# Optimization experiments

Hardware: AMD Instinct MI355X
Metric: run time of the kernel (lower is better)

The kernel has to match this reference:

```python
import jax, jax.numpy as jnp
import numpy as np

B, S, H = 1024, 128, 1024   # batch, seq_len, bert hidden size
E, HID, K, C = 16, 1024, 4, 3  # experts, expert hidden, top_k, num_classes
EPS = 1e-5


def _ln(x, g, b):
    mu = x.mean(-1, keepdims=True)
    var = ((x - mu) ** 2).mean(-1, keepdims=True)
    return (x - mu) / jnp.sqrt(var + EPS) * g + b


def setup_inputs() -> dict:
    key = jax.random.key(0)
    ks = jax.random.split(key, 24)
    n = lambda k, shape, s=0.02: jax.random.normal(k, shape, jnp.float32) * s
    return {
        "hidden_states": jax.random.normal(ks[0], (B, S, H), jnp.float32),
        # original BertClassificationHead
        "Wd": n(ks[1], (H, H)), "bd": jnp.zeros((H,), jnp.float32),
        "Wo": n(ks[2], (H, C)), "bo": jnp.zeros((C,), jnp.float32),
        # router
        "Wr": n(ks[3], (H, E)), "br": jnp.zeros((E,), jnp.float32),
        # stacked experts: Linear(H,HID) -> LN -> GELU -> Linear(HID,HID)
        "We1": n(ks[4], (E, H, HID)), "be1": jnp.zeros((E, HID), jnp.float32),
        "g1": jnp.ones((E, HID), jnp.float32), "beta1": jnp.zeros((E, HID), jnp.float32),
        "We2": n(ks[5], (E, HID, HID)), "be2": jnp.zeros((E, HID), jnp.float32),
        # expert_output_proj
        "Wp": n(ks[6], (HID, C)), "bp": jnp.zeros((C,), jnp.float32),
        # final_classifier: Linear(2C, C) -> LN -> ReLU -> Linear(C, C)
        "Wf1": n(ks[7], (2 * C, C)), "bf1": jnp.zeros((C,), jnp.float32),
        "gf": jnp.ones((C,), jnp.float32), "betaf": jnp.zeros((C,), jnp.float32),
        "Wf2": n(ks[8], (C, C)), "bf2": jnp.zeros((C,), jnp.float32),
    }


def reference(hidden_states, Wd, bd, Wo, bo, Wr, br, We1, be1, g1, beta1,
              We2, be2, Wp, bp, Wf1, bf1, gf, betaf, Wf2, bf2):
    cls = hidden_states[:, 0]                                   # [B,H]
    # original classifier head (dropout = identity in eval)
    original_logits = jnp.tanh(cls @ Wd + bd) @ Wo + bo         # [B,C]
    # router: top-k softmax scattered into dense [B,E] weights
    router_logits = cls @ Wr + br                               # [B,E]
    topk_vals, topk_idx = jax.lax.top_k(router_logits, K)
    topk_probs = jax.nn.softmax(topk_vals, axis=-1)
    routing_weights = jnp.zeros_like(router_logits).at[
        jnp.arange(cls.shape[0])[:, None], topk_idx].set(topk_probs)
    # experts consume mean-pooled sequence (MLPExpert mean over dim=1)
    m = hidden_states.mean(axis=1)                              # [B,H]
    h = jnp.einsum('bh,ehd->bed', m, We1) + be1                 # [B,E,HID]
    h = jax.nn.gelu(_ln(h, g1, beta1), approximate=False)
    h = jnp.einsum('bed,edf->bef', h, We2) + be2                # [B,E,HID]
    expert_logits = h @ Wp + bp                                 # [B,E,C]
    # weighted combine; routing_weights is zero for non-selected experts,
    # so this equals the sparse top-k dispatch of the original loop
    moe_output = jnp.einsum('be,bec->bc', routing_weights, expert_logits)
    combined = jnp.concatenate([original_logits, moe_output], axis=1)  # [B,2C]
    z = _ln(combined @ Wf1 + bf1, gf, betaf)
    return jax.nn.relu(z) @ Wf2 + bf2                           # [B,C]
```

## Files before the change

### kernel.cpp

```cpp
#include <hip/hip_runtime.h>
#include <math.h>

#define B_ 1024
#define S_ 128
#define H_ 1024
#define E_ 16
#define HID_ 1024
#define K_ 4
#define C_ 3
#define EPS_ 1e-5f

#define NB_MEAN 1024
#define NB_WC 4096
#define NB_RT 256
#define NB_BC 4
#define OFF_WC (NB_MEAN)
#define OFF_RT (OFF_WC + NB_WC)
#define OFF_BC (OFF_RT + NB_RT)
#define NB_PREP (OFF_BC + NB_BC)

typedef __attribute__((ext_vector_type(8))) __bf16 bf16x8;
typedef __attribute__((ext_vector_type(4))) float f32x4;
typedef __attribute__((ext_vector_type(4))) float fvec4;
typedef __attribute__((ext_vector_type(4))) unsigned short usvec4;
typedef __attribute__((ext_vector_type(8))) unsigned short usvec8;

__device__ __forceinline__ ushort bf16_rn(float f) {
  unsigned u = __float_as_uint(f);
  u += 0x7FFF + ((u >> 16) & 1);
  return (ushort)(u >> 16);
}
__device__ __forceinline__ float bf16_to_f(ushort h) {
  return __uint_as_float(((unsigned)h) << 16);
}
__device__ __forceinline__ void split2(float f, ushort& h, ushort& l) {
  h = bf16_rn(f);
  l = bf16_rn(f - bf16_to_f(h));
}
__device__ __forceinline__ void gload_lds16(const void* g, void* l) {
  __builtin_amdgcn_global_load_lds((const __attribute__((address_space(1))) void*)g,
                                   (__attribute__((address_space(3))) void*)l, 16, 0, 0);
}
#define DMA_DRAIN() do {                                  \
    asm volatile("s_waitcnt vmcnt(0)" ::: "memory");      \
    __builtin_amdgcn_sched_barrier(0);                    \
  } while (0)

__device__ __forceinline__ fvec4 nt_load4f(const float* p) {
  return __builtin_nontemporal_load((const fvec4*)p);
}
__device__ __forceinline__ void st4us(ushort* p, ushort a, ushort b, ushort c, ushort d) {
  usvec4 v; v.x = a; v.y = b; v.z = c; v.w = d;
  *(usvec4*)p = v;
}
__device__ __forceinline__ void nt_store1f(float* p, float v) {
  __builtin_nontemporal_store(v, p);
}
__device__ __forceinline__ void waveRed3(float& s0, float& s1, float& s2) {
#pragma unroll
  for (int off = 32; off; off >>= 1) {
    s0 += __shfl_down(s0, off); s1 += __shfl_down(s1, off); s2 += __shfl_down(s2, off);
  }
}

__global__ __launch_bounds__(256) void prep_kernel(
    const float* __restrict__ hs,
    const float* __restrict__ We2, const float* __restrict__ Wp, const float* __restrict__ bp,
    const float* __restrict__ Wr, const float* __restrict__ br,
    const float* __restrict__ be2,
    ushort* __restrict__ m_hi, ushort* __restrict__ m_lo,
    ushort* __restrict__ cls_hi, ushort* __restrict__ cls_lo,
    float* __restrict__ Wcomb, float* __restrict__ bcomb,
    int* __restrict__ topk_idx, float* __restrict__ topk_prob,
    int* __restrict__ counts, int* __restrict__ pairlist) {
  const int blk = blockIdx.x;
  const int tid = threadIdx.x;

  if (blk < NB_MEAN) {
    int gid = blk * 256 + tid;
    int b = gid >> 8;
    int h4 = (gid & 255) << 2;
    const float* p = hs + (size_t)b * S_ * H_ + h4;
    fvec4 v0 = nt_load4f(p);
    float sx = v0.x, sy = v0.y, sz = v0.z, sw = v0.w;
#pragma unroll 8
    for (int s = 1; s < S_; ++s) {
      fvec4 v = nt_load4f(p + (size_t)s * H_);
      sx += v.x; sy += v.y; sz += v.z; sw += v.w;
    }
    const float inv = 1.0f / (float)S_;
    float mv[4] = {sx * inv, sy * inv, sz * inv, sw * inv};
    float cv[4] = {v0.x, v0.y, v0.z, v0.w};
    ushort mh[4], ml[4], ch[4], cl[4];
#pragma unroll
    for (int i = 0; i < 4; ++i) { split2(mv[i], mh[i], ml[i]); split2(cv[i], ch[i], cl[i]); }
    size_t o = (size_t)b * H_ + h4;
    st4us(&m_hi[o], mh[0], mh[1], mh[2], mh[3]);
    st4us(&m_lo[o], ml[0], ml[1], ml[2], ml[3]);
    st4us(&cls_hi[o], ch[0], ch[1], ch[2], ch[3]);
    st4us(&cls_lo[o], cl[0], cl[1], cl[2], cl[3]);
  } else if (blk < OFF_RT) {
    const int row = (blk - OFF_WC) * 4 + (tid >> 6);
    const int lane = tid & 63;
    const float* wrp = We2 + (size_t)row * HID_;
    float s0 = 0, s1 = 0, s2 = 0;
#pragma unroll
    for (int it = 0; it < 4; ++it) {
      const int f0 = it * 256 + lane * 4;
      fvec4 v = nt_load4f(&wrp[f0]);
      s0 = fmaf(v.x, Wp[(f0 + 0) * 3 + 0], s0);
      s1 = fmaf(v.x, Wp[(f0 + 0) * 3 + 1], s1);
      s2 = fmaf(v.x, Wp[(f0 + 0) * 3 + 2], s2);
      s0 = fmaf(v.y, Wp[(f0 + 1) * 3 + 0], s0);
      s1 = fmaf(v.y, Wp[(f0 + 1) * 3 + 1], s1);
      s2 = fmaf(v.y, Wp[(f0 + 1) * 3 + 2], s2);
      s0 = fmaf(v.z, Wp[(f0 + 2) * 3 + 0], s0);
      s1 = fmaf(v.z, Wp[(f0 + 2) * 3 + 1], s1);
      s2 = fmaf(v.z, Wp[(f0 + 2) * 3 + 2], s2);
      s0 = fmaf(v.w, Wp[(f0 + 3) * 3 + 0], s0);
      s1 = fmaf(v.w, Wp[(f0 + 3) * 3 + 1], s1);
      s2 = fmaf(v.w, Wp[(f0 + 3) * 3 + 2], s2);
    }
    waveRed3(s0, s1, s2);
    if (lane == 0) {
      Wcomb[row * 3 + 0] = s0; Wcomb[row * 3 + 1] = s1; Wcomb[row * 3 + 2] = s2;
    }
  } else if (blk < OFF_BC) {
    const int lane = tid & 63;
    const int b = (blk - OFF_RT) * 4 + (tid >> 6);
    const float* cls = hs + (size_t)b * S_ * H_;
    const int e = lane & 15, part = lane >> 4;
    float sum = 0.0f;
    for (int i = part * 256; i < part * 256 + 256; ++i)
      sum = fmaf(cls[i], Wr[i * E_ + e], sum);
    sum += __shfl_down(sum, 32);
    sum += __shfl_down(sum, 16);
    float lg[E_];
#pragma unroll
    for (int i = 0; i < E_; ++i) lg[i] = __shfl(sum, i);
    if (lane == 0) {
      for (int i = 0; i < E_; ++i) lg[i] += br[i];
      int idx[K_]; float tv[K_];
      for (int k = 0; k < K_; ++k) {
        int bi = 0; float bv = -1e30f;
        for (int i = 0; i < E_; ++i) { if (lg[i] > bv) { bv = lg[i]; bi = i; } }
        idx[k] = bi; tv[k] = bv; lg[bi] = -1e30f;
      }
      float mx = tv[0], ssum = 0.0f, p[K_];
      for (int k = 0; k < K_; ++k) { p[k] = expf(tv[k] - mx); ssum += p[k]; }
      for (int k = 0; k < K_; ++k) {
        p[k] /= ssum;
        topk_idx[b * K_ + k] = idx[k];
        topk_prob[b * K_ + k] = p[k];
        int pos = atomicAdd(&counts[idx[k]], 1);
        pairlist[idx[k] * B_ + pos] = b * K_ + k;
      }
    }
  } else {
    const int e = (blk - OFF_BC) * 4 + (tid >> 6);
    const int lane = tid & 63;
    const float* wrp = be2 + (size_t)e * HID_;
    float s0 = 0, s1 = 0, s2 = 0;
    for (int f = lane; f < HID_; f += 64) {
      float v = wrp[f];
      s0 = fmaf(v, Wp[f * 3 + 0], s0);
      s1 = fmaf(v, Wp[f * 3 + 1], s1);
      s2 = fmaf(v, Wp[f * 3 + 2], s2);
    }
    waveRed3(s0, s1, s2);
    if (lane == 0) {
      bcomb[e * 3 + 0] = s0 + bp[0]; bcomb[e * 3 + 1] = s1 + bp[1]; bcomb[e * 3 + 2] = s2 + bp[2];
    }
  }
}

__global__ __launch_bounds__(512) void gemm_mega(
    const ushort* __restrict__ m_hi, const ushort* __restrict__ m_lo,
    const ushort* __restrict__ cls_hi, const ushort* __restrict__ cls_lo,
    const float* __restrict__ Wd, const float* __restrict__ We1,
    const int* __restrict__ counts, const int* __restrict__ pairlist,
    float* __restrict__ tA, float* __restrict__ tB,
    float* __restrict__ h1A, float* __restrict__ h1B) {
  __shared__ __align__(16) ushort ldsAh0[4096], ldsAl0[4096], ldsBh0[4096], ldsBl0[4096];
  __shared__ __align__(16) ushort ldsAh1[4096], ldsAl1[4096], ldsBh1[4096], ldsBl1[4096];
  const int z = blockIdx.z;
  const int tid = threadIdx.x;
  const int lane = tid & 63, w = tid >> 6;
  const int mt = blockIdx.y >> 1, kh = blockIdx.y & 1;
  const int m0 = mt * 128, n0 = blockIdx.x * 128;
  const int kbase = kh * 512;
  int n_e;
  if (z == 16) n_e = B_;
  else { n_e = counts[z]; if (m0 >= n_e) return; }

  const ushort* srcp[4];
  ushort* dstA0 = nullptr; ushort* dstA1 = nullptr;
  const float* bbase[2];
  int bsub[2];
  const int halfq = w & 1;
  if (w < 4) {
    const int warr = w >> 1;
    dstA0 = (warr == 0) ? ldsAh0 : ldsAl0;
    dstA1 = (warr == 0) ? ldsAh1 : ldsAl1;
    const ushort* sbase;
    if (z == 16) sbase = (warr == 0) ? cls_hi : cls_lo;
    else         sbase = (warr == 0) ? m_hi  : m_lo;
#pragma unroll
    for (int sl = 0; sl < 4; ++sl) {
      int s = halfq * 4 + sl;
      int r = m0 + s * 16 + (lane & 15);
      if (z != 16) {
        if (r >= n_e) r = n_e - 1;
        r = pairlist[z * B_ + r] >> 2;
      }
      srcp[sl] = sbase + (size_t)r * H_ + ((lane >> 4) << 3);
    }
  } else {
    const float* Wfp = (z == 16) ? Wd : (We1 + (size_t)z * H_ * HID_);
#pragma unroll
    for (int sl = 0; sl < 2; ++sl) {
      int s = (w - 4) * 2 + sl;
      bsub[sl] = s;
      int col = n0 + s * 16 + (lane & 15);
      bbase[sl] = Wfp + col + (size_t)(lane >> 4) * 8 * HID_;
    }
  }

  const int wr = w >> 2, wc = w & 3;
  f32x4 acc[4][2] = {};

  auto stageA = [&](int kofs, ushort* dst) {
#pragma unroll
    for (int sl = 0; sl < 4; ++sl)
      gload_lds16(srcp[sl] + kofs, dst + (halfq * 4 + sl) * 512);
  };
  auto stageB = [&](int kofs, ushort* dBh, ushort* dBl) {
#pragma unroll
    for (int sl = 0; sl < 2; ++sl) {
      const float* bp = bbase[sl] + (size_t)kofs * HID_;
      float f[8];
#pragma unroll
      for (int j = 0; j < 8; ++j) f[j] = bp[(size_t)j * HID_];
      usvec8 vh, vl;
#pragma unroll
      for (int j = 0; j < 8; ++j) {
        ushort hi, lo;
        split2(f[j], hi, lo);
        vh[j] = hi; vl[j] = lo;
      }
      const int off = bsub[sl] * 512 + lane * 8;
      *(usvec8*)&dBh[off] = vh;
      *(usvec8*)&dBl[off] = vl;
    }
  };
  auto stage_buf0 = [&](int kofs) {
    if (w < 4) stageA(kofs, dstA0);
    else stageB(kofs, ldsBh0, ldsBl0);
  };
  auto stage_buf1 = [&](int kofs) {
    if (w < 4) stageA(kofs, dstA1);
    else stageB(kofs, ldsBh1, ldsBl1);
  };
  auto compute = [&](const ushort* Ah, const ushort* Al,
                     const ushort* Bh, const ushort* Bl) {
    bf16x8 ah[4], al[4], bh[2], bl[2];
#pragma unroll
    for (int i = 0; i < 4; ++i) {
      int off = (wr * 4 + i) * 512 + lane * 8;
      ah[i] = *(const bf16x8*)&Ah[off];
      al[i] = *(const bf16x8*)&Al[off];
    }
#pragma unroll
    for (int j = 0; j < 2; ++j) {
      int off = (wc * 2 + j) * 512 + lane * 8;
      bh[j] = *(const bf16x8*)&Bh[off];
      bl[j] = *(const bf16x8*)&Bl[off];
    }
#pragma unroll
    for (int i = 0; i < 4; ++i)
#pragma unroll
      for (int j = 0; j < 2; ++j) {
        acc[i][j] = __builtin_amdgcn_mfma_f32_16x16x32_bf16(ah[i], bh[j], acc[i][j], 0, 0, 0);
        acc[i][j] = __builtin_amdgcn_mfma_f32_16x16x32_bf16(ah[i], bl[j], acc[i][j], 0, 0, 0);
        acc[i][j] = __builtin_amdgcn_mfma_f32_16x16x32_bf16(al[i], bh[j], acc[i][j], 0, 0, 0);
      }
  };

  stage_buf0(kbase);
  DMA_DRAIN();
  __syncthreads();

#pragma unroll 1
  for (int tt = 0; tt < 8; ++tt) {
    const int t0 = tt * 2;
    stage_buf1(kbase + (t0 + 1) * 32);
    compute(ldsAh0, ldsAl0, ldsBh0, ldsBl0);
    DMA_DRAIN();
    __syncthreads();
    if (tt < 7) stage_buf0(kbase + (t0 + 2) * 32);
    compute(ldsAh1, ldsAl1, ldsBh1, ldsBl1);
    DMA_DRAIN();
    __syncthreads();
  }

  const int lr = (lane >> 4) << 2, lc = lane & 15;
  if (z == 16) {
    float* tp = kh ? tB : tA;
#pragma unroll
    for (int i = 0; i < 4; ++i) {
      int row = m0 + wr * 64 + i * 16 + lr;
#pragma unroll
      for (int j = 0; j < 2; ++j) {
        int col = n0 + wc * 32 + j * 16 + lc;
#pragma unroll
        for (int r = 0; r < 4; ++r)
          nt_store1f(&tp[(size_t)(row + r) * H_ + col], acc[i][j][r]);
      }
    }
  } else {
    float* hp = kh ? h1B : h1A;
#pragma unroll
    for (int i = 0; i < 4; ++i) {
      int pr[4]; bool ok[4];
#pragma unroll
      for (int r = 0; r < 4; ++r) {
        int li = m0 + wr * 64 + i * 16 + lr + r;
        ok[r] = li < n_e;
        pr[r] = pairlist[z * B_ + (ok[r] ? li : n_e - 1)];
      }
#pragma unroll
      for (int j = 0; j < 2; ++j) {
        int col = n0 + wc * 32 + j * 16 + lc;
#pragma unroll
        for (int r = 0; r < 4; ++r)
          if (ok[r]) nt_store1f(&hp[(size_t)pr[r] * HID_ + col], acc[i][j][r]);
      }
    }
  }
}

__global__ __launch_bounds__(256) void epi_kernel(
    const float* __restrict__ tA, const float* __restrict__ tB,
    const float* __restrict__ bd,
    const float* __restrict__ Wo, const float* __restrict__ bo,
    const float* __restrict__ h1A, const float* __restrict__ h1B,
    const float* __restrict__ be1,
    const float* __restrict__ g1, const float* __restrict__ beta1,
    const int* __restrict__ topk_idx, const float* __restrict__ topk_prob,
    const float* __restrict__ Wcomb, const float* __restrict__ bcomb,
    const float* __restrict__ Wf1, const float* __restrict__ bf1,
    const float* __restrict__ gf, const float* __restrict__ betaf,
    const float* __restrict__ Wf2, const float* __restrict__ bf2,
    float* __restrict__ out) {
  const int b = blockIdx.x;
  const int tid = threadIdx.x;
  const int w = tid >> 6, lane = tid & 63;
  __shared__ float sCtr[4][3];
  __shared__ float sOl[4][3];

  const int pair = b * K_ + w;
  const int e = topk_idx[pair];
  const float prob = topk_prob[pair];
  const float* hrA = h1A + (size_t)pair * HID_;
  const float* hrB = h1B + (size_t)pair * HID_;
  const float* ber = be1 + (size_t)e * HID_;
  float x[4][4];
#pragma unroll
  for (int q = 0; q < 4; ++q) {
    const int d = q * 256 + lane * 4;
    fvec4 a = nt_load4f(&hrA[d]);
    fvec4 bq = nt_load4f(&hrB[d]);
    float4 be = *(const float4*)&ber[d];
    x[q][0] = a.x + bq.x + be.x; x[q][1] = a.y + bq.y + be.y;
    x[q][2] = a.z + bq.z + be.z; x[q][3] = a.w + bq.w + be.w;
  }
  float s = 0;
#pragma unroll
  for (int q = 0; q < 4; ++q) s += x[q][0] + x[q][1] + x[q][2] + x[q][3];
#pragma unroll
  for (int off = 32; off; off >>= 1) s += __shfl_down(s, off);
  const float mu = __shfl(s, 0) * (1.0f / HID_);
  float sq = 0;
#pragma unroll
  for (int q = 0; q < 4; ++q)
#pragma unroll
    for (int i = 0; i < 4; ++i) {
      float d = x[q][i] - mu;
      sq += d * d;
    }
#pragma unroll
  for (int off = 32; off; off >>= 1) sq += __shfl_down(sq, off);
  const float inv = 1.0f / sqrtf(__shfl(sq, 0) * (1.0f / HID_) + EPS_);
  float c0 = 0, c1 = 0, c2 = 0;
#pragma unroll
  for (int q = 0; q < 4; ++q) {
    const int d = q * 256 + lane * 4;
    float4 gg = *(const float4*)&g1[(size_t)e * HID_ + d];
    float4 bb = *(const float4*)&beta1[(size_t)e * HID_ + d];
    float gv[4] = {gg.x, gg.y, gg.z, gg.w};
    float bv[4] = {bb.x, bb.y, bb.z, bb.w};
#pragma unroll
    for (int i = 0; i < 4; ++i) {
      float v = (x[q][i] - mu) * inv * gv[i] + bv[i];
      v = 0.5f * v * (1.0f + erff(v * 0.70710678118654752440f));
      const float* wc = &Wcomb[(size_t)(e * HID_ + d + i) * 3];
      c0 = fmaf(v, wc[0], c0); c1 = fmaf(v, wc[1], c1); c2 = fmaf(v, wc[2], c2);
    }
  }
  waveRed3(c0, c1, c2);
  if (lane == 0) {
    sCtr[w][0] = prob * (c0 + bcomb[e * 3 + 0]);
    sCtr[w][1] = prob * (c1 + bcomb[e * 3 + 1]);
    sCtr[w][2] = prob * (c2 + bcomb[e * 3 + 2]);
  }

  {
    const int h0 = w * 256 + lane * 4;
    fvec4 ta = nt_load4f(&tA[(size_t)b * H_ + h0]);
    fvec4 tb = nt_load4f(&tB[(size_t)b * H_ + h0]);
    float4 bdv = *(const float4*)&bd[h0];
    float tvv[4] = {tanhf(ta.x + tb.x + bdv.x), tanhf(ta.y + tb.y + bdv.y),
                    tanhf(ta.z + tb.z + bdv.z), tanhf(ta.w + tb.w + bdv.w)};
    float o0 = 0, o1 = 0, o2 = 0;
#pragma unroll
    for (int i = 0; i < 4; ++i) {
      const float* wo = &Wo[(size_t)(h0 + i) * 3];
      o0 = fmaf(tvv[i], wo[0], o0); o1 = fmaf(tvv[i], wo[1], o1); o2 = fmaf(tvv[i], wo[2], o2);
    }
    waveRed3(o0, o1, o2);
    if (lane == 0) { sOl[w][0] = o0; sOl[w][1] = o1; sOl[w][2] = o2; }
  }
  __syncthreads();

  if (tid == 0) {
    float comb[6];
#pragma unroll
    for (int c = 0; c < 3; ++c) {
      comb[c] = sOl[0][c] + sOl[1][c] + sOl[2][c] + sOl[3][c] + bo[c];
      comb[3 + c] = sCtr[0][c] + sCtr[1][c] + sCtr[2][c] + sCtr[3][c];
    }
    float z[3];
#pragma unroll
    for (int c = 0; c < 3; ++c) {
      float sv = bf1[c];
#pragma unroll
      for (int i = 0; i < 6; ++i) sv = fmaf(comb[i], Wf1[i * 3 + c], sv);
      z[c] = sv;
    }
    float mu3 = (z[0] + z[1] + z[2]) * (1.0f / 3.0f);
    float v0 = z[0] - mu3, v1 = z[1] - mu3, v2 = z[2] - mu3;
    float var = (v0 * v0 + v1 * v1 + v2 * v2) * (1.0f / 3.0f);
    float inv3 = 1.0f / sqrtf(var + EPS_);
    float r[3];
#pragma unroll
    for (int c = 0; c < 3; ++c) {
      float zz = (z[c] - mu3) * inv3 * gf[c] + betaf[c];
      r[c] = zz > 0.0f ? zz : 0.0f;
    }
#pragma unroll
    for (int c = 0; c < 3; ++c) {
      float sv = bf2[c];
#pragma unroll
      for (int i = 0; i < 3; ++i) sv = fmaf(r[i], Wf2[i * 3 + c], sv);
      out[b * 3 + c] = sv;
    }
  }
}

extern "C" void kernel_launch(void* const* d_in, const int* in_sizes, int n_in,
                              void* d_out, int out_size, void* d_ws, size_t ws_size,
                              hipStream_t stream) {
  const float* hs    = (const float*)d_in[0];
  const float* Wd    = (const float*)d_in[1];
  const float* bd    = (const float*)d_in[2];
  const float* Wo    = (const float*)d_in[3];
  const float* bo    = (const float*)d_in[4];
  const float* Wr    = (const float*)d_in[5];
  const float* br    = (const float*)d_in[6];
  const float* We1   = (const float*)d_in[7];
  const float* be1   = (const float*)d_in[8];
  const float* g1    = (const float*)d_in[9];
  const float* beta1 = (const float*)d_in[10];
  const float* We2   = (const float*)d_in[11];
  const float* be2   = (const float*)d_in[12];
  const float* Wp    = (const float*)d_in[13];
  const float* bp    = (const float*)d_in[14];
  const float* Wf1   = (const float*)d_in[15];
  const float* bf1   = (const float*)d_in[16];
  const float* gf    = (const float*)d_in[17];
  const float* betaf = (const float*)d_in[18];
  const float* Wf2   = (const float*)d_in[19];
  const float* bf2   = (const float*)d_in[20];
  float* out = (float*)d_out;

  char* w = (char*)d_ws;
  size_t off = 0;
  auto alloc = [&](size_t bytes) {
    void* p = w + off;
    off = (off + bytes + 255) & ~(size_t)255;
    return p;
  };
  ushort* m_hi   = (ushort*)alloc((size_t)B_ * H_ * 2);
  ushort* m_lo   = (ushort*)alloc((size_t)B_ * H_ * 2);
  ushort* cls_hi = (ushort*)alloc((size_t)B_ * H_ * 2);
  ushort* cls_lo = (ushort*)alloc((size_t)B_ * H_ * 2);
  float* ws_tA   = (float*)alloc((size_t)B_ * H_ * 4);
  float* ws_tB   = (float*)alloc((size_t)B_ * H_ * 4);
  float* ws_h1A  = (float*)alloc((size_t)B_ * K_ * HID_ * 4);
  float* ws_h1B  = (float*)alloc((size_t)B_ * K_ * HID_ * 4);
  float* ws_wc   = (float*)alloc((size_t)E_ * HID_ * 3 * 4);
  float* ws_bc   = (float*)alloc(E_ * 3 * 4);
  float* ws_prob = (float*)alloc(B_ * K_ * 4);
  int* ws_idx = (int*)alloc(B_ * K_ * 4);
  int* ws_cnt = (int*)alloc(E_ * 4);
  int* ws_pl  = (int*)alloc(E_ * B_ * 4);
  if (off > ws_size) return;

  hipMemsetAsync(ws_cnt, 0, E_ * sizeof(int), stream);

  prep_kernel<<<NB_PREP, 256, 0, stream>>>(hs, We2, Wp, bp, Wr, br, be2,
                                           m_hi, m_lo, cls_hi, cls_lo,
                                           ws_wc, ws_bc,
                                           ws_idx, ws_prob, ws_cnt, ws_pl);
  gemm_mega<<<dim3(8, 16, 17), 512, 0, stream>>>(m_hi, m_lo, cls_hi, cls_lo,
                                                 Wd, We1, ws_cnt, ws_pl,
                                                 ws_tA, ws_tB, ws_h1A, ws_h1B);
  epi_kernel<<<B_, 256, 0, stream>>>(ws_tA, ws_tB, bd, Wo, bo, ws_h1A, ws_h1B, be1,
                                     g1, beta1, ws_idx, ws_prob, ws_wc, ws_bc,
                                     Wf1, bf1, gf, betaf, Wf2, bf2, out);
}
```

Measured before the change: 231.3 us.

## Move CLS dense GEMM into prep kernel, reading hidden_states directly

The CLS×Wd head GEMM moves out of the expert GEMM kernel into the prep kernel. Its 128 blocks read fp32 CLS rows straight from hidden_states and split them to bf16 hi/lo in-kernel, so the cls_hi/cls_lo staging buffers are no longer written or read. Running it in the same launch as the memory-bound mean reduction lets MFMA work overlap the streaming. The prep kernel now uses 512-thread blocks with half the block count, and large-LDS GEMM blocks share the grid with light reduction blocks, which may lower occupancy for the mean pass.

```diff
diff --git a/kernel.cpp b/kernel.cpp
--- a/kernel.cpp
+++ b/kernel.cpp
@@ -10,14 +10,16 @@
 #define C_ 3
 #define EPS_ 1e-5f
 
-#define NB_MEAN 1024
-#define NB_WC 4096
-#define NB_RT 256
-#define NB_BC 4
-#define OFF_WC (NB_MEAN)
+#define NB_CLSG 128
+#define OFF_MEAN (NB_CLSG)
+#define NB_MEAN 512
+#define OFF_WC (OFF_MEAN + NB_MEAN)
+#define NB_WC 2048
 #define OFF_RT (OFF_WC + NB_WC)
+#define NB_RT 128
 #define OFF_BC (OFF_RT + NB_RT)
-#define NB_PREP (OFF_BC + NB_BC)
+#define NB_BC 2
+#define NB_P1 (OFF_BC + NB_BC)
 
 typedef __attribute__((ext_vector_type(8))) __bf16 bf16x8;
 typedef __attribute__((ext_vector_type(4))) float f32x4;
@@ -63,21 +65,137 @@
   }
 }
 
-__global__ __launch_bounds__(256) void prep_kernel(
+__global__ __launch_bounds__(512) void phase1_kernel(
     const float* __restrict__ hs,
+    const float* __restrict__ Wd,
     const float* __restrict__ We2, const float* __restrict__ Wp, const float* __restrict__ bp,
     const float* __restrict__ Wr, const float* __restrict__ br,
     const float* __restrict__ be2,
     ushort* __restrict__ m_hi, ushort* __restrict__ m_lo,
-    ushort* __restrict__ cls_hi, ushort* __restrict__ cls_lo,
     float* __restrict__ Wcomb, float* __restrict__ bcomb,
     int* __restrict__ topk_idx, float* __restrict__ topk_prob,
-    int* __restrict__ counts, int* __restrict__ pairlist) {
+    int* __restrict__ counts, int* __restrict__ pairlist,
+    float* __restrict__ tA, float* __restrict__ tB) {
+  __shared__ __align__(16) ushort ldsAh0[4096], ldsAl0[4096], ldsBh0[4096], ldsBl0[4096];
+  __shared__ __align__(16) ushort ldsAh1[4096], ldsAl1[4096], ldsBh1[4096], ldsBl1[4096];
   const int blk = blockIdx.x;
   const int tid = threadIdx.x;
-
-  if (blk < NB_MEAN) {
-    int gid = blk * 256 + tid;
+  const int w = tid >> 6, lane = tid & 63;
+
+  if (blk < NB_CLSG) {
+    const int n0 = (blk & 7) * 128;
+    const int yy = blk >> 3;
+    const int mt = yy >> 1, kh = yy & 1;
+    const int m0 = mt * 128;
+    const int kbase = kh * 512;
+    const float* sbase[2];
+    size_t kstride;
+    int subs0;
+    if (w < 4) {
+      kstride = 1;
+      subs0 = w * 2;
+#pragma unroll
+      for (int sl = 0; sl < 2; ++sl) {
+        int s = subs0 + sl;
+        int b = m0 + s * 16 + (lane & 15);
+        sbase[sl] = hs + (size_t)b * (S_ * H_) + ((lane >> 4) << 3);
+      }
+    } else {
+      kstride = H_;
+      subs0 = (w - 4) * 2;
+#pragma unroll
+      for (int sl = 0; sl < 2; ++sl) {
+        int s = subs0 + sl;
+        int col = n0 + s * 16 + (lane & 15);
+        sbase[sl] = Wd + col + (size_t)((lane >> 4) << 3) * H_;
+      }
+    }
+    const int wr = w >> 2, wc = w & 3;
+    f32x4 acc[4][2] = {};
+
+    auto stage = [&](int kofs, ushort* dAh, ushort* dAl, ushort* dBh, ushort* dBl) {
+      ushort* dh = (w < 4) ? dAh : dBh;
+      ushort* dl = (w < 4) ? dAl : dBl;
+#pragma unroll
+      for (int sl = 0; sl < 2; ++sl) {
+        const float* p = sbase[sl] + (size_t)kofs * kstride;
+        float f[8];
+        if (w < 4) {
+          fvec4 v0 = nt_load4f(p);
+          fvec4 v1 = nt_load4f(p + 4);
+          f[0] = v0.x; f[1] = v0.y; f[2] = v0.z; f[3] = v0.w;
+          f[4] = v1.x; f[5] = v1.y; f[6] = v1.z; f[7] = v1.w;
+        } else {
+#pragma unroll
+          for (int j = 0; j < 8; ++j) f[j] = p[(size_t)j * H_];
+        }
+        usvec8 vh, vl;
+#pragma unroll
+        for (int j = 0; j < 8; ++j) {
+          ushort hi, lo;
+          split2(f[j], hi, lo);
+          vh[j] = hi; vl[j] = lo;
+        }
+        const int off = (subs0 + sl) * 512 + lane * 8;
+        *(usvec8*)&dh[off] = vh;
+        *(usvec8*)&dl[off] = vl;
+      }
+    };
+    auto compute = [&](const ushort* Ah, const ushort* Al,
+                       const ushort* Bh, const ushort* Bl) {
+      bf16x8 ah[4], al[4], bh[2], bl[2];
+#pragma unroll
+      for (int i = 0; i < 4; ++i) {
+        int off = (wr * 4 + i) * 512 + lane * 8;
+        ah[i] = *(const bf16x8*)&Ah[off];
+        al[i] = *(const bf16x8*)&Al[off];
+      }
+#pragma unroll
+      for (int j = 0; j < 2; ++j) {
+        int off = (wc * 2 + j) * 512 + lane * 8;
+        bh[j] = *(const bf16x8*)&Bh[off];
+        bl[j] = *(const bf16x8*)&Bl[off];
+      }
+#pragma unroll
+      for (int i = 0; i < 4; ++i)
+#pragma unroll
+        for (int j = 0; j < 2; ++j) {
+          acc[i][j] = __builtin_amdgcn_mfma_f32_16x16x32_bf16(ah[i], bh[j], acc[i][j], 0, 0, 0);
+          acc[i][j] = __builtin_amdgcn_mfma_f32_16x16x32_bf16(ah[i], bl[j], acc[i][j], 0, 0, 0);
+          acc[i][j] = __builtin_amdgcn_mfma_f32_16x16x32_bf16(al[i], bh[j], acc[i][j], 0, 0, 0);
+        }
+    };
+
+    stage(kbase, ldsAh0, ldsAl0, ldsBh0, ldsBl0);
+    DMA_DRAIN();
+    __syncthreads();
+#pragma unroll 1
+    for (int tt = 0; tt < 8; ++tt) {
+      const int t0 = tt * 2;
+      stage(kbase + (t0 + 1) * 32, ldsAh1, ldsAl1, ldsBh1, ldsBl1);
+      compute(ldsAh0, ldsAl0, ldsBh0, ldsBl0);
+      DMA_DRAIN();
+      __syncthreads();
+      if (tt < 7) stage(kbase + (t0 + 2) * 32, ldsAh0, ldsAl0, ldsBh0, ldsBl0);
+      compute(ldsAh1, ldsAl1, ldsBh1, ldsBl1);
+      DMA_DRAIN();
+      __syncthreads();
+    }
+    const int lr = (lane >> 4) << 2, lc = lane & 15;
+    float* tp = kh ? tB : tA;
+#pragma unroll
+    for (int i = 0; i < 4; ++i) {
+      int row = m0 + wr * 64 + i * 16 + lr;
+#pragma unroll
+      for (int j = 0; j < 2; ++j) {
+        int col = n0 + wc * 32 + j * 16 + lc;
+#pragma unroll
+        for (int r = 0; r < 4; ++r)
+          nt_store1f(&tp[(size_t)(row + r) * H_ + col], acc[i][j][r]);
+      }
+    }
+  } else if (blk < OFF_WC) {
+    int gid = (blk - OFF_MEAN) * 512 + tid;
     int b = gid >> 8;
     int h4 = (gid & 255) << 2;
     const float* p = hs + (size_t)b * S_ * H_ + h4;
@@ -90,18 +208,14 @@
     }
     const float inv = 1.0f / (float)S_;
     float mv[4] = {sx * inv, sy * inv, sz * inv, sw * inv};
-    float cv[4] = {v0.x, v0.y, v0.z, v0.w};
-    ushort mh[4], ml[4], ch[4], cl[4];
-#pragma unroll
-    for (int i = 0; i < 4; ++i) { split2(mv[i], mh[i], ml[i]); split2(cv[i], ch[i], cl[i]); }
+    ushort mh[4], ml[4];
+#pragma unroll
+    for (int i = 0; i < 4; ++i) split2(mv[i], mh[i], ml[i]);
     size_t o = (size_t)b * H_ + h4;
     st4us(&m_hi[o], mh[0], mh[1], mh[2], mh[3]);
     st4us(&m_lo[o], ml[0], ml[1], ml[2], ml[3]);
-    st4us(&cls_hi[o], ch[0], ch[1], ch[2], ch[3]);
-    st4us(&cls_lo[o], cl[0], cl[1], cl[2], cl[3]);
   } else if (blk < OFF_RT) {
-    const int row = (blk - OFF_WC) * 4 + (tid >> 6);
-    const int lane = tid & 63;
+    const int row = (blk - OFF_WC) * 8 + w;
     const float* wrp = We2 + (size_t)row * HID_;
     float s0 = 0, s1 = 0, s2 = 0;
 #pragma unroll
@@ -126,8 +240,7 @@
       Wcomb[row * 3 + 0] = s0; Wcomb[row * 3 + 1] = s1; Wcomb[row * 3 + 2] = s2;
     }
   } else if (blk < OFF_BC) {
-    const int lane = tid & 63;
-    const int b = (blk - OFF_RT) * 4 + (tid >> 6);
+    const int b = (blk - OFF_RT) * 8 + w;
     const float* cls = hs + (size_t)b * S_ * H_;
     const int e = lane & 15, part = lane >> 4;
     float sum = 0.0f;
@@ -157,8 +270,7 @@
       }
     }
   } else {
-    const int e = (blk - OFF_BC) * 4 + (tid >> 6);
-    const int lane = tid & 63;
+    const int e = (blk - OFF_BC) * 8 + w;
     const float* wrp = be2 + (size_t)e * HID_;
     float s0 = 0, s1 = 0, s2 = 0;
     for (int f = lane; f < HID_; f += 64) {
@@ -174,12 +286,10 @@
   }
 }
 
-__global__ __launch_bounds__(512) void gemm_mega(
+__global__ __launch_bounds__(512) void expert_gemm(
     const ushort* __restrict__ m_hi, const ushort* __restrict__ m_lo,
-    const ushort* __restrict__ cls_hi, const ushort* __restrict__ cls_lo,
-    const float* __restrict__ Wd, const float* __restrict__ We1,
+    const float* __restrict__ We1,
     const int* __restrict__ counts, const int* __restrict__ pairlist,
-    float* __restrict__ tA, float* __restrict__ tB,
     float* __restrict__ h1A, float* __restrict__ h1B) {
   __shared__ __align__(16) ushort ldsAh0[4096], ldsAl0[4096], ldsBh0[4096], ldsBl0[4096];
   __shared__ __align__(16) ushort ldsAh1[4096], ldsAl1[4096], ldsBh1[4096], ldsBl1[4096];
@@ -189,9 +299,8 @@
   const int mt = blockIdx.y >> 1, kh = blockIdx.y & 1;
   const int m0 = mt * 128, n0 = blockIdx.x * 128;
   const int kbase = kh * 512;
-  int n_e;
-  if (z == 16) n_e = B_;
-  else { n_e = counts[z]; if (m0 >= n_e) return; }
+  const int n_e = counts[z];
+  if (m0 >= n_e) return;
 
   const ushort* srcp[4];
   ushort* dstA0 = nullptr; ushort* dstA1 = nullptr;
@@ -202,27 +311,23 @@
     const int warr = w >> 1;
     dstA0 = (warr == 0) ? ldsAh0 : ldsAl0;
     dstA1 = (warr == 0) ? ldsAh1 : ldsAl1;
-    const ushort* sbase;
-    if (z == 16) sbase = (warr == 0) ? cls_hi : cls_lo;
-    else         sbase = (warr == 0) ? m_hi  : m_lo;
+    const ushort* sbase = (warr == 0) ? m_hi : m_lo;
 #pragma unroll
     for (int sl = 0; sl < 4; ++sl) {
       int s = halfq * 4 + sl;
       int r = m0 + s * 16 + (lane & 15);
-      if (z != 16) {
-        if (r >= n_e) r = n_e - 1;
-        r = pairlist[z * B_ + r] >> 2;
-      }
+      if (r >= n_e) r = n_e - 1;
+      r = pairlist[z * B_ + r] >> 2;
       srcp[sl] = sbase + (size_t)r * H_ + ((lane >> 4) << 3);
     }
   } else {
-    const float* Wfp = (z == 16) ? Wd : (We1 + (size_t)z * H_ * HID_);
+    const float* Wfp = We1 + (size_t)z * H_ * HID_;
 #pragma unroll
     for (int sl = 0; sl < 2; ++sl) {
       int s = (w - 4) * 2 + sl;
       bsub[sl] = s;
       int col = n0 + s * 16 + (lane & 15);
-      bbase[sl] = Wfp + col + (size_t)(lane >> 4) * 8 * HID_;
+      bbase[sl] = Wfp + col + (size_t)((lane >> 4) << 3) * HID_;
     }
   }
 
@@ -289,7 +394,6 @@
   stage_buf0(kbase);
   DMA_DRAIN();
   __syncthreads();
-
 #pragma unroll 1
   for (int tt = 0; tt < 8; ++tt) {
     const int t0 = tt * 2;
@@ -304,37 +408,22 @@
   }
 
   const int lr = (lane >> 4) << 2, lc = lane & 15;
-  if (z == 16) {
-    float* tp = kh ? tB : tA;
-#pragma unroll
-    for (int i = 0; i < 4; ++i) {
-      int row = m0 + wr * 64 + i * 16 + lr;
-#pragma unroll
-      for (int j = 0; j < 2; ++j) {
-        int col = n0 + wc * 32 + j * 16 + lc;
-#pragma unroll
-        for (int r = 0; r < 4; ++r)
-          nt_store1f(&tp[(size_t)(row + r) * H_ + col], acc[i][j][r]);
-      }
-    }
-  } else {
-    float* hp = kh ? h1B : h1A;
-#pragma unroll
-    for (int i = 0; i < 4; ++i) {
-      int pr[4]; bool ok[4];
-#pragma unroll
-      for (int r = 0; r < 4; ++r) {
-        int li = m0 + wr * 64 + i * 16 + lr + r;
-        ok[r] = li < n_e;
-        pr[r] = pairlist[z * B_ + (ok[r] ? li : n_e - 1)];
-      }
-#pragma unroll
-      for (int j = 0; j < 2; ++j) {
-        int col = n0 + wc * 32 + j * 16 + lc;
-#pragma unroll
-        for (int r = 0; r < 4; ++r)
-          if (ok[r]) nt_store1f(&hp[(size_t)pr[r] * HID_ + col], acc[i][j][r]);
-      }
+  float* hp = kh ? h1B : h1A;
+#pragma unroll
+  for (int i = 0; i < 4; ++i) {
+    int pr[4]; bool ok[4];
+#pragma unroll
+    for (int r = 0; r < 4; ++r) {
+      int li = m0 + wr * 64 + i * 16 + lr + r;
+      ok[r] = li < n_e;
+      pr[r] = pairlist[z * B_ + (ok[r] ? li : n_e - 1)];
+    }
+#pragma unroll
+    for (int j = 0; j < 2; ++j) {
+      int col = n0 + wc * 32 + j * 16 + lc;
+#pragma unroll
+      for (int r = 0; r < 4; ++r)
+        if (ok[r]) nt_store1f(&hp[(size_t)pr[r] * HID_ + col], acc[i][j][r]);
     }
   }
 }
@@ -502,8 +591,6 @@
   };
   ushort* m_hi   = (ushort*)alloc((size_t)B_ * H_ * 2);
   ushort* m_lo   = (ushort*)alloc((size_t)B_ * H_ * 2);
-  ushort* cls_hi = (ushort*)alloc((size_t)B_ * H_ * 2);
-  ushort* cls_lo = (ushort*)alloc((size_t)B_ * H_ * 2);
   float* ws_tA   = (float*)alloc((size_t)B_ * H_ * 4);
   float* ws_tB   = (float*)alloc((size_t)B_ * H_ * 4);
   float* ws_h1A  = (float*)alloc((size_t)B_ * K_ * HID_ * 4);
@@ -518,13 +605,12 @@
 
   hipMemsetAsync(ws_cnt, 0, E_ * sizeof(int), stream);
 
-  prep_kernel<<<NB_PREP, 256, 0, stream>>>(hs, We2, Wp, bp, Wr, br, be2,
-                                           m_hi, m_lo, cls_hi, cls_lo,
-                                           ws_wc, ws_bc,
-                                           ws_idx, ws_prob, ws_cnt, ws_pl);
-  gemm_mega<<<dim3(8, 16, 17), 512, 0, stream>>>(m_hi, m_lo, cls_hi, cls_lo,
-                                                 Wd, We1, ws_cnt, ws_pl,
-                                                 ws_tA, ws_tB, ws_h1A, ws_h1B);
+  phase1_kernel<<<NB_P1, 512, 0, stream>>>(hs, Wd, We2, Wp, bp, Wr, br, be2,
+                                           m_hi, m_lo, ws_wc, ws_bc,
+                                           ws_idx, ws_prob, ws_cnt, ws_pl,
+                                           ws_tA, ws_tB);
+  expert_gemm<<<dim3(8, 16, 16), 512, 0, stream>>>(m_hi, m_lo, We1, ws_cnt, ws_pl,
+                                                   ws_h1A, ws_h1B);
   epi_kernel<<<B_, 256, 0, stream>>>(ws_tA, ws_tB, bd, Wo, bo, ws_h1A, ws_h1B, be1,
                                      g1, beta1, ws_idx, ws_prob, ws_wc, ws_bc,
                                      Wf1, bf1, gf, betaf, Wf2, bf2, out);
```

Result: no change. 235.2 us (+1.7%).
